# Optimization experiments

Hardware: AMD Instinct MI355X
Metric: run time of the kernel (lower is better)

## Reference

```python
import jax, jax.numpy as jnp
import numpy as np

B, N, F, H = 4, 1024, 1024, 16
D = F // H  # head_dim = 64


def setup_inputs() -> dict:
    key = jax.random.key(0)
    ks = jax.random.split(key, 12)
    s = 1.0 / np.sqrt(F)
    return {
        "feature_map": jax.random.normal(ks[0], (B, N, F), jnp.float32),
        "scene_token": jax.random.normal(ks[1], (B, F), jnp.float32),
        "relation_matrix": jax.random.normal(ks[2], (2 * N, 2 * N), jnp.float32) * 0.05,
        "Wq": jax.random.normal(ks[3], (F, F), jnp.float32) * s,
        "bq": jnp.zeros((F,), jnp.float32),
        "Wk": jax.random.normal(ks[4], (F, F), jnp.float32) * s,
        "bk": jnp.zeros((F,), jnp.float32),
        "Wv": jax.random.normal(ks[5], (F, F), jnp.float32) * s,
        "bv": jnp.zeros((F,), jnp.float32),
        "Wo": jax.random.normal(ks[6], (F, F), jnp.float32) * s,
        "bo": jnp.zeros((F,), jnp.float32),
    }


def reference(feature_map, scene_token, relation_matrix, Wq, bq, Wk, bk, Wv, bv, Wo, bo):
    b, n, f = feature_map.shape
    # scene token broadcast to n copies, concatenated -> [b, 2n, f]
    scene = jnp.broadcast_to(scene_token[:, None, :], (b, n, f))
    x = jnp.concatenate([scene, feature_map], axis=1)  # [b, 2n, f]
    q = (x @ Wq.T + bq).reshape(b, -1, H, D)
    k = (x @ Wk.T + bk).reshape(b, -1, H, D)
    v = (x @ Wv.T + bv).reshape(b, -1, H, D)
    scores = jnp.einsum("bqhd,bkhd->bhqk", q, k) / jnp.sqrt(jnp.float32(D))
    scores = scores + relation_matrix[None, None, :, :]
    weights = jax.nn.softmax(scores, axis=-1)
    attn = jnp.einsum("bhqk,bkhd->bqhd", weights, v).reshape(b, -1, f)
    return attn @ Wo.T + bo
```

## Files before the change

kernel.cpp:

```cpp
#include <hip/hip_runtime.h>
#include <hip/hip_bf16.h>
#include <cstdint>

typedef __hip_bfloat16 bf16;
typedef __attribute__((ext_vector_type(8))) short short8;
typedef __attribute__((ext_vector_type(4))) short short4v;
typedef __attribute__((ext_vector_type(4))) float f32x4;
typedef __attribute__((ext_vector_type(2))) unsigned int uint2v;

#define MFMA16(a, b, c) __builtin_amdgcn_mfma_f32_16x16x32_bf16((a), (b), (c), 0, 0, 0)

__device__ __forceinline__ void gl2lds16(const void* g, void* l) {
  __builtin_amdgcn_global_load_lds(
      (const __attribute__((address_space(1))) unsigned int*)g,
      (__attribute__((address_space(3))) unsigned int*)l,
      16, 0, 0);
}

__device__ __forceinline__ unsigned int pkcvt(float a, float b) {
  unsigned int r;
  asm("v_cvt_pk_bf16_f32 %0, %1, %2" : "=v"(r) : "v"(a), "v"(b));
  return r;
}

// ... 16 lines not shown
#endif
}

__device__ __forceinline__ uint2v plswap16(unsigned a, unsigned b) {
#if __has_builtin(__builtin_amdgcn_permlane16_swap)
  return __builtin_amdgcn_permlane16_swap(a, b, false, false);
#else
  const unsigned ax = __shfl_xor((int)a, 16), bx = __shfl_xor((int)b, 16);
  const bool hi = (threadIdx.x & 16) != 0;
  uint2v r;
  r[0] = hi ? bx : a;
  r[1] = hi ? b : ax;
  return r;
#endif
}

template <int V> struct IC { static constexpr int value = V; };

template <int WRITE_BF16, int REMAP>
__global__ __launch_bounds__(256) void gemm_bt(
    const bf16* __restrict__ A, const bf16* __restrict__ Bt,
    const float* __restrict__ bias, bf16* __restrict__ outb,
    float* __restrict__ outf, int M, int N, int K) {
  __shared__ bf16 sA[128 * 64];
  __shared__ bf16 sB[128 * 64];
  const int tid = threadIdx.x, w = tid >> 6, lane = tid & 63;
  const int n16 = lane & 15, quad = lane >> 4;
  const int mBase = blockIdx.y * 128, nBase = blockIdx.x * 128;
  const int wr = w >> 1, wc = w & 1;

  f32x4 acc[4][4];
#pragma unroll
  for (int mi = 0; mi < 4; mi++)
#pragma unroll
    for (int ni = 0; ni < 4; ni++) acc[mi][ni] = (f32x4){0.f, 0.f, 0.f, 0.f};

  const bf16* ag[4];
  const bf16* bg[4];
#pragma unroll
  for (int i = 0; i < 4; i++) {
    const int e = (i * 256 + tid) * 8;
    const int row = e >> 6, c0 = e & 63;
    const int col = c0 ^ ((row & 7) << 3);
    ag[i] = A + (size_t)(mBase + row) * K + col;
    bg[i] = Bt + (size_t)(nBase + row) * K + col;
  }
  const int u = (quad * 16) ^ ((n16 & 7) << 4);
  const int a0 = (wr * 64 + n16) * 128 + u;
// ... 6 lines not shown
#pragma unroll
    for (int i = 0; i < 4; i++) {
      gl2lds16(ag[i] + k0, sA + i * 2048 + w * 512);
      gl2lds16(bg[i] + k0, sB + i * 2048 + w * 512);
    }
    __syncthreads();

#pragma unroll
    for (int kk = 0; kk < 2; kk++) {
      short8 af[4], bfg[4];
#pragma unroll
      for (int t = 0; t < 4; t++) {
        af[t] = *(const short8*)(sAB + (a0 ^ (kk << 6)) + t * 2048);
        bfg[t] = *(const short8*)(sBB + (b0 ^ (kk << 6)) + t * 2048);
      }
#pragma unroll
      for (int mi = 0; mi < 4; mi++)
#pragma unroll
        for (int ni = 0; ni < 4; ni++)
          acc[mi][ni] = MFMA16(af[mi], bfg[ni], acc[mi][ni]);
    }
  }

#pragma unroll
  for (int mi = 0; mi < 4; mi++)
#pragma unroll
    for (int ni = 0; ni < 4; ni++)
#pragma unroll
      for (int r = 0; r < 4; r++) {
        const int row = mBase + wr * 64 + mi * 16 + quad * 4 + r;
        const int col = nBase + wc * 64 + ni * 16 + n16;
        const size_t orow =
            REMAP ? (size_t)((row >> 10) * 2048 + 1024 + (row & 1023))
                  : (size_t)row;
        const float v = acc[mi][ni][r] + bias[col];
        if (WRITE_BF16)
          outb[orow * N + col] = __float2bfloat16(v);
        else
          outf[orow * N + col] = v;
      }
}

__global__ __launch_bounds__(256) void flash_feat(
    const bf16* __restrict__ qkv, const float* __restrict__ relf,
    bf16* __restrict__ attn, const float* __restrict__ lR1) {
  constexpr int S = 2048, R3 = 3072;
  __shared__ __align__(16) char smem[32768];
  bf16* const sK = (bf16*)smem;
  char* const sVtB = smem + 16384;

  const int tid = threadIdx.x, w = tid >> 6, lane = tid & 63;
  const int n16 = lane & 15, quad = lane >> 4;
  const int bh = blockIdx.x >> 3;
  const int qt = 8 + (blockIdx.x & 7);
  const int h = bh & 15, b = bh >> 4;
  const int qb = qt * 128 + w * 32;
  const size_t rowbase = (size_t)b * S;
  const size_t krow0 = rowbase + 1024;
  const float SC = 0.125f * 1.44269504f;
  const size_t TADV = (size_t)64 * R3;

  short8 qf[2][2];
#pragma unroll
  for (int mi = 0; mi < 2; mi++) {
    const bf16* qp = qkv + (rowbase + qb + mi * 16 + n16) * R3 + h * 64;
#pragma unroll
    for (int c = 0; c < 2; c++)
      qf[mi][c] = *(const short8*)(qp + c * 32 + quad * 8);
  }

  f32x4 ot[4][2];
#pragma unroll
  for (int nc = 0; nc < 4; nc++)
#pragma unroll
    for (int mi = 0; mi < 2; mi++) ot[nc][mi] = (f32x4){0.f, 0.f, 0.f, 0.f};
  float l_lane[2] = {0.f, 0.f};

  const bf16* kg0;
  const bf16* kg1;
  {
    const int e0 = tid * 8;
    const int e1i = (256 + tid) * 8;
    const int k0r = e0 >> 6, c00 = e0 & 63;
    const int k1r = e1i >> 6, c01 = e1i & 63;
    kg0 = qkv + (krow0 + k0r) * R3 + 1024 + h * 64 + (c00 ^ ((k0r & 7) << 3));
    kg1 = qkv + (krow0 + k1r) * R3 + 1024 + h * 64 + (c01 ^ ((k1r & 7) << 3));
  }
  const int kldsoff = w * 512;

  const int kb0 = n16 * 128 + ((quad * 16) ^ ((n16 & 7) << 4));
  const int kb1 = kb0 ^ 64;
  const char* const sKB = (const char*)sK;

  const int kp = lane & 31;
  const int vd0 = w * 16 + (lane >> 5) * 8;
  const int kp4 = kp * 4;
  const bf16* vp = qkv + (krow0 + 2 * kp) * R3 + 2048 + h * 64 + vd0;

  const int vb0 = 128 * n16 + ((16 * quad) ^ ((n16 & 7) << 4));
  const int vb1 = vb0 ^ 64;

  short8 v0, v1;
  auto vstage = [&](int bufbyte) {
    const unsigned* a1 = (const unsigned*)&v1;
    const unsigned* a0 = (const unsigned*)&v0;
#pragma unroll
    for (int j = 0; j < 4; j++) {
      const unsigned lo = __builtin_amdgcn_perm(a1[j], a0[j], 0x05040100u);
      const unsigned hi = __builtin_amdgcn_perm(a1[j], a0[j], 0x07060302u);
      *(unsigned*)(sVtB + bufbyte + 128 * (vd0 + 2 * j) + (kp4 ^ ((2 * j) << 4))) = lo;
      *(unsigned*)(sVtB + bufbyte + 128 * (vd0 + 2 * j + 1) + (kp4 ^ ((2 * j + 1) << 4))) = hi;
    }
  };

  gl2lds16(kg0, sK + kldsoff);
  gl2lds16(kg1, sK + kldsoff + 2048);
  kg0 += TADV;
  kg1 += TADV;

  v0 = *(const short8*)vp;
  v1 = *(const short8*)(vp + R3);
  vstage(0);
  vp += TADV;
  v0 = *(const short8*)vp;
  v1 = *(const short8*)(vp + R3);
  vp += TADV;

  float4 rv[8];
  const float4* rpA = (const float4*)relf +
                      (size_t)(qt * 32 + 16) * 2048 + w * 512 + lane;
  const float4* rpB = rpA + 256;
#pragma unroll
  for (int j = 0; j < 4; j++) {
    rv[j] = rpA[j * 64];
    rv[4 + j] = rpB[j * 64];
  }
  rpA += 2048;
  rpB += 2048;

  auto step = [&](auto curc, bool dodma, bool dovpf) {
    constexpr int CUR = decltype(curc)::value;
    constexpr int NXT = CUR ^ 1;
    __syncthreads();

    if (dodma) {
      gl2lds16(kg0, sK + NXT * 4096 + kldsoff);
      kg0 += TADV;
      gl2lds16(kg1, sK + NXT * 4096 + kldsoff + 2048);
      kg1 += TADV;
      vstage(NXT * 8192);
    }

#pragma unroll
    for (int kc = 0; kc < 2; kc++) {
      f32x4 st[2][2];
#pragma unroll
      for (int t2 = 0; t2 < 2; t2++) {
        const int kt4 = 2 * kc + t2;
        short8 kf[2];
        kf[0] = *(const short8*)(sKB + CUR * 8192 + kt4 * 2048 + kb0);
        kf[1] = *(const short8*)(sKB + CUR * 8192 + kt4 * 2048 + kb1);
#pragma unroll
        for (int mi = 0; mi < 2; mi++) {
          f32x4 z = (f32x4){0.f, 0.f, 0.f, 0.f};
          z = MFMA16(kf[0], qf[mi][0], z);
          z = MFMA16(kf[1], qf[mi][1], z);
          st[t2][mi] = z;
        }
      }
      if (kc == 0 && dovpf) {
        v0 = *(const short8*)vp;
        v1 = *(const short8*)(vp + R3);
        vp += TADV;
      }
      short8 pb[2];
#pragma unroll
      for (int mi = 0; mi < 2; mi++) {
        float acc = 0.f;
        unsigned d[2][2];
#pragma unroll
        for (int t2 = 0; t2 < 2; t2++) {
          const float4 rr = rv[mi * 4 + 2 * kc + t2];
          float p0 = __builtin_amdgcn_exp2f(fmaf(st[t2][mi][0], SC, rr.x));
          float p1 = __builtin_amdgcn_exp2f(fmaf(st[t2][mi][1], SC, rr.y));
          float p2 = __builtin_amdgcn_exp2f(fmaf(st[t2][mi][2], SC, rr.z));
          float p3 = __builtin_amdgcn_exp2f(fmaf(st[t2][mi][3], SC, rr.w));
          acc += (p0 + p1) + (p2 + p3);
          d[t2][0] = pkcvt(p0, p1);
          d[t2][1] = pkcvt(p2, p3);
        }
        l_lane[mi] += acc;
        const uint2v e0 = plswap32(d[0][0], d[1][0]);
        const uint2v e1 = plswap32(d[0][1], d[1][1]);
        const uint2v f0 = plswap16(e0[0], e0[1]);
        const uint2v f1 = plswap16(e1[0], e1[1]);
        union { short8 s; unsigned u[4]; } P;
        P.u[0] = f0[0]; P.u[1] = f1[0]; P.u[2] = f0[1]; P.u[3] = f1[1];
        pb[mi] = P.s;
      }
      if (kc == 1 && dodma) {
#pragma unroll
        for (int j = 0; j < 4; j++) {
          rv[j] = rpA[j * 64];
          rv[4 + j] = rpB[j * 64];
        }
        rpA += 2048;
        rpB += 2048;
      }
      short8 va[4];
#pragma unroll
      for (int nc = 0; nc < 4; nc++)
        va[nc] = *(const short8*)(sVtB + CUR * 8192 + 2048 * nc +
                                  (kc ? vb1 : vb0));
#pragma unroll
      for (int nc = 0; nc < 4; nc++)
#pragma unroll
        for (int mi = 0; mi < 2; mi++)
          ot[nc][mi] = MFMA16(va[nc], pb[mi], ot[nc][mi]);
    }
  };

#pragma unroll 1
  for (int t = 0; t < 8; t++) {
    const bool g = (t < 7);
    step(IC<0>{}, true, g);
    step(IC<1>{}, g, g);
  }

  {
    const bf16* kscp = qkv + rowbase * R3 + 1024 + h * 64 + quad * 8;
    const short8 ks0 = *(const short8*)(kscp);
    const short8 ks1 = *(const short8*)(kscp + 32);
    float e1v[2];
#pragma unroll
    for (int mi = 0; mi < 2; mi++) {
      float ss = 0.f;
#pragma unroll
      for (int j = 0; j < 8; j++) {
        ss = fmaf(b2f((unsigned short)qf[mi][0][j]), b2f((unsigned short)ks0[j]), ss);
        ss = fmaf(b2f((unsigned short)qf[mi][1][j]), b2f((unsigned short)ks1[j]), ss);
      }
      ss += __shfl_xor(ss, 16);
      ss += __shfl_xor(ss, 32);
      const float lr = lR1[qb + mi * 16 + n16];
      e1v[mi] = __builtin_amdgcn_exp2f(fmaf(ss, SC, lr));
      if (quad == 0) l_lane[mi] += e1v[mi];
    }
    const bf16* vscp = qkv + rowbase * R3 + 2048 + h * 64;
#pragma unroll
    for (int nc = 0; nc < 4; nc++) {
      const int d0 = nc * 16 + quad * 4;
      const uint2 vv = *(const uint2*)(vscp + d0);
      const float w0 = b2f((unsigned short)(vv.x & 0xffff));
      const float w1 = b2f((unsigned short)(vv.x >> 16));
      const float w2 = b2f((unsigned short)(vv.y & 0xffff));
      const float w3 = b2f((unsigned short)(vv.y >> 16));
#pragma unroll
      for (int mi = 0; mi < 2; mi++) {
        ot[nc][mi][0] = fmaf(e1v[mi], w0, ot[nc][mi][0]);
        ot[nc][mi][1] = fmaf(e1v[mi], w1, ot[nc][mi][1]);
        ot[nc][mi][2] = fmaf(e1v[mi], w2, ot[nc][mi][2]);
        ot[nc][mi][3] = fmaf(e1v[mi], w3, ot[nc][mi][3]);
      }
    }
  }

  float inv[2];
#pragma unroll
  for (int mi = 0; mi < 2; mi++) {
    float l = l_lane[mi];
    l += __shfl_xor(l, 16);
    l += __shfl_xor(l, 32);
    inv[mi] = 1.0f / l;
  }
  __syncthreads();
  bf16* const sEp = (bf16*)smem + w * (32 * 72);
#pragma unroll
  for (int mi = 0; mi < 2; mi++)
#pragma unroll
    for (int nc = 0; nc < 4; nc++) {
      uint2 pk;
      pk.x = pkcvt(ot[nc][mi][0] * inv[mi], ot[nc][mi][1] * inv[mi]);
      pk.y = pkcvt(ot[nc][mi][2] * inv[mi], ot[nc][mi][3] * inv[mi]);
      *(uint2*)(&sEp[(mi * 16 + n16) * 72 + nc * 16 + quad * 4]) = pk;
    }
#pragma unroll
  for (int t = 0; t < 4; t++) {
    const int row = t * 8 + (lane >> 3);
    const int dcol = (lane & 7) * 8;
    const short8 vrow = *(const short8*)(&sEp[row * 72 + dcol]);
    *(short8*)(attn + (rowbase + qb + row) * 1024 + h * 64 + dcol) = vrow;
  }
}

__global__ __launch_bounds__(256) void flash_scene(
    const bf16* __restrict__ qkv, const float* __restrict__ relf,
    bf16* __restrict__ attn, const float* __restrict__ lR1,
    const float* __restrict__ ssf, const float* __restrict__ ssc) {
  constexpr int S = 2048, R3 = 3072;
  __shared__ __align__(16) char smem[18432];
  char* const sVtB = smem;

  const int tid = threadIdx.x, w = tid >> 6, lane = tid & 63;
  const int n16 = lane & 15, quad = lane >> 4;
  const int bh = blockIdx.x >> 3;
  const int qt = blockIdx.x & 7;
  const int h = bh & 15, b = bh >> 4;
  const int qb = qt * 128 + w * 32;
  const size_t rowbase = (size_t)b * S;
  const size_t krow0 = rowbase + 1024;
  const size_t TADV = (size_t)64 * R3;

  f32x4 ot[4][2];
#pragma unroll
  for (int nc = 0; nc < 4; nc++)
#pragma unroll
    for (int mi = 0; mi < 2; mi++) ot[nc][mi] = (f32x4){0.f, 0.f, 0.f, 0.f};
  float l_lane[2] = {0.f, 0.f};

  const int kp = lane & 31;
  const int vd0 = w * 16 + (lane >> 5) * 8;
  const int kp4 = kp * 4;
  const bf16* vp = qkv + (krow0 + 2 * kp) * R3 + 2048 + h * 64 + vd0;

  const int vb0 = 128 * n16 + ((16 * quad) ^ ((n16 & 7) << 4));
  const int vb1 = vb0 ^ 64;

  const float* ssp = ssf + (size_t)bh * 1024 + quad * 4;

  short8 v0, v1;
  auto vstage = [&](int bufbyte) {
    const unsigned* a1 = (const unsigned*)&v1;
    const unsigned* a0 = (const unsigned*)&v0;
#pragma unroll
    for (int j = 0; j < 4; j++) {
      const unsigned lo = __builtin_amdgcn_perm(a1[j], a0[j], 0x05040100u);
      const unsigned hi = __builtin_amdgcn_perm(a1[j], a0[j], 0x07060302u);
      *(unsigned*)(sVtB + bufbyte + 128 * (vd0 + 2 * j) + (kp4 ^ ((2 * j) << 4))) = lo;
      *(unsigned*)(sVtB + bufbyte + 128 * (vd0 + 2 * j + 1) + (kp4 ^ ((2 * j + 1) << 4))) = hi;
    }
  };

  v0 = *(const short8*)vp;
  v1 = *(const short8*)(vp + R3);
  vstage(0);
  vp += TADV;
  v0 = *(const short8*)vp;
  v1 = *(const short8*)(vp + R3);
  vp += TADV;

  float4 rv[8];
  const float4* rpA = (const float4*)relf +
                      (size_t)(qt * 32 + 16) * 2048 + w * 512 + lane;
  const float4* rpB = rpA + 256;
#pragma unroll
  for (int j = 0; j < 4; j++) {
    rv[j] = rpA[j * 64];
    rv[4 + j] = rpB[j * 64];
  }
  rpA += 2048;
  rpB += 2048;

  auto step = [&](auto curc, bool dodma, bool dovpf) {
    constexpr int CUR = decltype(curc)::value;
    constexpr int NXT = CUR ^ 1;
    __syncthreads();
    if (dodma) vstage(NXT * 8192);

#pragma unroll
    for (int kc = 0; kc < 2; kc++) {
      float4 ssq[2];
      ssq[0] = *(const float4*)(ssp + (2 * kc + 0) * 16);
      ssq[1] = *(const float4*)(ssp + (2 * kc + 1) * 16);
      if (kc == 0 && dovpf) {
        v0 = *(const short8*)vp;
        v1 = *(const short8*)(vp + R3);
        vp += TADV;
      }
      short8 pb[2];
#pragma unroll
      for (int mi = 0; mi < 2; mi++) {
        float acc = 0.f;
        unsigned d[2][2];
#pragma unroll
        for (int t2 = 0; t2 < 2; t2++) {
          const float4 rr = rv[mi * 4 + 2 * kc + t2];
          float p0 = __builtin_amdgcn_exp2f(ssq[t2].x + rr.x);
          float p1 = __builtin_amdgcn_exp2f(ssq[t2].y + rr.y);
          float p2 = __builtin_amdgcn_exp2f(ssq[t2].z + rr.z);
          float p3 = __builtin_amdgcn_exp2f(ssq[t2].w + rr.w);
          acc += (p0 + p1) + (p2 + p3);
          d[t2][0] = pkcvt(p0, p1);
          d[t2][1] = pkcvt(p2, p3);
        }
        l_lane[mi] += acc;
        const uint2v e0 = plswap32(d[0][0], d[1][0]);
        const uint2v e1 = plswap32(d[0][1], d[1][1]);
        const uint2v f0 = plswap16(e0[0], e0[1]);
        const uint2v f1 = plswap16(e1[0], e1[1]);
        union { short8 s; unsigned u[4]; } P;
        P.u[0] = f0[0]; P.u[1] = f1[0]; P.u[2] = f0[1]; P.u[3] = f1[1];
        pb[mi] = P.s;
      }
      if (kc == 1 && dodma) {
#pragma unroll
        for (int j = 0; j < 4; j++) {
          rv[j] = rpA[j * 64];
          rv[4 + j] = rpB[j * 64];
        }
        rpA += 2048;
        rpB += 2048;
      }
      short8 va[4];
#pragma unroll
      for (int nc = 0; nc < 4; nc++)
        va[nc] = *(const short8*)(sVtB + CUR * 8192 + 2048 * nc +
                                  (kc ? vb1 : vb0));
#pragma unroll
      for (int nc = 0; nc < 4; nc++)
#pragma unroll
        for (int mi = 0; mi < 2; mi++)
          ot[nc][mi] = MFMA16(va[nc], pb[mi], ot[nc][mi]);
    }
    ssp += 64;
  };

#pragma unroll 1
  for (int t = 0; t < 8; t++) {
    const bool g = (t < 7);
    step(IC<0>{}, true, g);
    step(IC<1>{}, g, g);
  }

  {
    const float sscv = ssc[bh];
    float e1v[2];
#pragma unroll
    for (int mi = 0; mi < 2; mi++) {
      const float lr = lR1[qb + mi * 16 + n16];
      e1v[mi] = __builtin_amdgcn_exp2f(sscv + lr);
      if (quad == 0) l_lane[mi] += e1v[mi];
    }
    const bf16* vscp = qkv + rowbase * R3 + 2048 + h * 64;
#pragma unroll
    for (int nc = 0; nc < 4; nc++) {
      const int d0 = nc * 16 + quad * 4;
      const uint2 vv = *(const uint2*)(vscp + d0);
      const float w0 = b2f((unsigned short)(vv.x & 0xffff));
      const float w1 = b2f((unsigned short)(vv.x >> 16));
      const float w2 = b2f((unsigned short)(vv.y & 0xffff));
      const float w3 = b2f((unsigned short)(vv.y >> 16));
#pragma unroll
      for (int mi = 0; mi < 2; mi++) {
        ot[nc][mi][0] = fmaf(e1v[mi], w0, ot[nc][mi][0]);
        ot[nc][mi][1] = fmaf(e1v[mi], w1, ot[nc][mi][1]);
        ot[nc][mi][2] = fmaf(e1v[mi], w2, ot[nc][mi][2]);
        ot[nc][mi][3] = fmaf(e1v[mi], w3, ot[nc][mi][3]);
      }
    }
  }

  float inv[2];
#pragma unroll
  for (int mi = 0; mi < 2; mi++) {
    float l = l_lane[mi];
    l += __shfl_xor(l, 16);
    l += __shfl_xor(l, 32);
    inv[mi] = 1.0f / l;
  }
  __syncthreads();
  bf16* const sEp = (bf16*)smem + w * (32 * 72);
#pragma unroll
  for (int mi = 0; mi < 2; mi++)
#pragma unroll
    for (int nc = 0; nc < 4; nc++) {
      uint2 pk;
      pk.x = pkcvt(ot[nc][mi][0] * inv[mi], ot[nc][mi][1] * inv[mi]);
      pk.y = pkcvt(ot[nc][mi][2] * inv[mi], ot[nc][mi][3] * inv[mi]);
      *(uint2*)(&sEp[(mi * 16 + n16) * 72 + nc * 16 + quad * 4]) = pk;
    }
#pragma unroll
  for (int t = 0; t < 4; t++) {
    const int row = t * 8 + (lane >> 3);
    const int dcol = (lane & 7) * 8;
    const short8 vrow = *(const short8*)(&sEp[row * 72 + dcol]);
    *(short8*)(attn + (rowbase + qb + row) * 1024 + h * 64 + dcol) = vrow;
  }
}

__global__ void prep_main(const float* __restrict__ fm, const float* __restrict__ Wq,
                          const float* __restrict__ Wk, const float* __restrict__ Wv,
                          const float* __restrict__ Wo, const float* __restrict__ bq,
                          const float* __restrict__ bk, const float* __restrict__ bv,
                          bf16* __restrict__ wW, bf16* __restrict__ wWo,
                          float* __restrict__ bC, bf16* __restrict__ x) {
  const int blk = blockIdx.x;
  if (blk < 4096) {
    const int sel = blk >> 10;
    const int i = (((blk & 1023) * 256) + threadIdx.x) * 4;
    const float* src = (sel == 0) ? Wq : (sel == 1) ? Wk : (sel == 2) ? Wv : Wo;
    bf16* dst = (sel < 3) ? (wW + ((size_t)sel << 20) + i) : (wWo + i);
    const float4 v = *(const float4*)(src + i);
    dst[0] = __float2bfloat16(v.x);
    dst[1] = __float2bfloat16(v.y);
    dst[2] = __float2bfloat16(v.z);
    dst[3] = __float2bfloat16(v.w);
    if (blk == 0) {
      for (int z = threadIdx.x; z < 3072; z += 256)
        bC[z] = (z < 1024) ? bq[z] : (z < 2048) ? bk[z - 1024] : bv[z - 2048];
// ... 127 lines not shown
  const float* bo    = (const float*)d_in[10];
  float* out = (float*)d_out;

  char* ws = (char*)d_ws;
  bf16* x    = (bf16*)(ws);
  float* relf = (float*)(ws);
  bf16* qkv  = (bf16*)(ws + (16u << 20));
  bf16* attn = (bf16*)(ws + (64u << 20));
  bf16* wW   = (bf16*)(ws + (80u << 20));
  bf16* wWo  = (bf16*)(ws + (86u << 20));
  float* bC  = (float*)(ws + (88u << 20));
  float* lR1 = (float*)(ws + (88u << 20) + 16384);
  bf16* sqv  = (bf16*)(ws + (88u << 20) + 32768);
  float* ssf = (float*)(ws + (88u << 20) + 65536);
  float* ssc = (float*)(ws + (88u << 20) + 65536 + 262144);

  prep_main<<<8192, 256, 0, stream>>>(fm, Wq, Wk, Wv, Wo, bq, bk, bv,
                                      wW, wWo, bC, x);
  scene_qkv<<<768, 256, 0, stream>>>(scene, wW, bC, sqv, qkv);
  gemm_bt<1, 1><<<dim3(24, 32), 256, 0, stream>>>(x, wW, bC, qkv, nullptr,
                                                  4096, 3072, 1024);
  sscomp<<<4100, 256, 0, stream>>>(qkv, sqv, ssf, ssc);
  prep_relr1<<<2048, 256, 0, stream>>>(rel, relf, lR1);
  flash_feat<<<512, 256, 0, stream>>>(qkv, relf, attn, lR1);
  flash_scene<<<512, 256, 0, stream>>>(qkv, relf, attn, lR1, ssf, ssc);
  gemm_bt<0, 0><<<dim3(8, 64), 256, 0, stream>>>(attn, wWo, bo, nullptr, out,
                                                 8192, 1024, 1024);
}
```

Measured before the change: 255.0 us.

## Stage GEMM epilogue through LDS for coalesced stores; merge flash kernels into one launch

The GEMM epilogue now writes the accumulator tile into shared memory and then stores whole rows with 16-byte vector writes, replacing scattered scalar global stores. The shared buffer is enlarged to hold the padded output tile. The feature-query and scene-query attention kernels are merged into one 1024-block launch that branches on block index. This removes one launch and its tail, and lets the two halves share the GPU at the same time. The cost is extra LDS traffic and barriers in the epilogue, plus higher register and LDS pressure in the merged kernel.

After: 260.6 us. 1.02x slower.

```diff
diff --git a/kernel.cpp b/kernel.cpp
--- a/kernel.cpp
+++ b/kernel.cpp
@@ -62,8 +62,9 @@
     const bf16* __restrict__ A, const bf16* __restrict__ Bt,
     const float* __restrict__ bias, bf16* __restrict__ outb,
     float* __restrict__ outf, int M, int N, int K) {
-  __shared__ bf16 sA[128 * 64];
-  __shared__ bf16 sB[128 * 64];
+  __shared__ __align__(16) char smemRaw[34816];
+  bf16* const sA = (bf16*)smemRaw;
+  bf16* const sB = (bf16*)(smemRaw + 16384);
   const int tid = threadIdx.x, w = tid >> 6, lane = tid & 63;
   const int n16 = lane & 15, quad = lane >> 4;
   const int mBase = blockIdx.y * 128, nBase = blockIdx.x * 128;
@@ -116,469 +117,499 @@
     }
   }
 
-#pragma unroll
-  for (int mi = 0; mi < 4; mi++)
-#pragma unroll
-    for (int ni = 0; ni < 4; ni++)
-#pragma unroll
-      for (int r = 0; r < 4; r++) {
-        const int row = mBase + wr * 64 + mi * 16 + quad * 4 + r;
-        const int col = nBase + wc * 64 + ni * 16 + n16;
-        const size_t orow =
-            REMAP ? (size_t)((row >> 10) * 2048 + 1024 + (row & 1023))
-                  : (size_t)row;
-        const float v = acc[mi][ni][r] + bias[col];
-        if (WRITE_BF16)
-          outb[orow * N + col] = __float2bfloat16(v);
-        else
-          outf[orow * N + col] = v;
-      }
-}
-
-__global__ __launch_bounds__(256) void flash_feat(
-    const bf16* __restrict__ qkv, const float* __restrict__ relf,
-    bf16* __restrict__ attn, const float* __restrict__ lR1) {
-  constexpr int S = 2048, R3 = 3072;
-  __shared__ __align__(16) char smem[32768];
-  bf16* const sK = (bf16*)smem;
-  char* const sVtB = smem + 16384;
-
-  const int tid = threadIdx.x, w = tid >> 6, lane = tid & 63;
-  const int n16 = lane & 15, quad = lane >> 4;
-  const int bh = blockIdx.x >> 3;
-  const int qt = 8 + (blockIdx.x & 7);
-  const int h = bh & 15, b = bh >> 4;
-  const int qb = qt * 128 + w * 32;
-  const size_t rowbase = (size_t)b * S;
-  const size_t krow0 = rowbase + 1024;
-  const float SC = 0.125f * 1.44269504f;
-  const size_t TADV = (size_t)64 * R3;
-
-  short8 qf[2][2];
-#pragma unroll
-  for (int mi = 0; mi < 2; mi++) {
-    const bf16* qp = qkv + (rowbase + qb + mi * 16 + n16) * R3 + h * 64;
-#pragma unroll
-    for (int c = 0; c < 2; c++)
-      qf[mi][c] = *(const short8*)(qp + c * 32 + quad * 8);
-  }
-
-  f32x4 ot[4][2];
-#pragma unroll
-  for (int nc = 0; nc < 4; nc++)
-#pragma unroll
-    for (int mi = 0; mi < 2; mi++) ot[nc][mi] = (f32x4){0.f, 0.f, 0.f, 0.f};
-  float l_lane[2] = {0.f, 0.f};
-
-  const bf16* kg0;
-  const bf16* kg1;
-  {
-    const int e0 = tid * 8;
-    const int e1i = (256 + tid) * 8;
-    const int k0r = e0 >> 6, c00 = e0 & 63;
-    const int k1r = e1i >> 6, c01 = e1i & 63;
-    kg0 = qkv + (krow0 + k0r) * R3 + 1024 + h * 64 + (c00 ^ ((k0r & 7) << 3));
-    kg1 = qkv + (krow0 + k1r) * R3 + 1024 + h * 64 + (c01 ^ ((k1r & 7) << 3));
-  }
-  const int kldsoff = w * 512;
-
-  const int kb0 = n16 * 128 + ((quad * 16) ^ ((n16 & 7) << 4));
-  const int kb1 = kb0 ^ 64;
-  const char* const sKB = (const char*)sK;
-
-  const int kp = lane & 31;
-  const int vd0 = w * 16 + (lane >> 5) * 8;
-  const int kp4 = kp * 4;
-  const bf16* vp = qkv + (krow0 + 2 * kp) * R3 + 2048 + h * 64 + vd0;
-
-  const int vb0 = 128 * n16 + ((16 * quad) ^ ((n16 & 7) << 4));
-  const int vb1 = vb0 ^ 64;
-
-  short8 v0, v1;
-  auto vstage = [&](int bufbyte) {
-    const unsigned* a1 = (const unsigned*)&v1;
-    const unsigned* a0 = (const unsigned*)&v0;
-#pragma unroll
-    for (int j = 0; j < 4; j++) {
-      const unsigned lo = __builtin_amdgcn_perm(a1[j], a0[j], 0x05040100u);
-      const unsigned hi = __builtin_amdgcn_perm(a1[j], a0[j], 0x07060302u);
-      *(unsigned*)(sVtB + bufbyte + 128 * (vd0 + 2 * j) + (kp4 ^ ((2 * j) << 4))) = lo;
-      *(unsigned*)(sVtB + bufbyte + 128 * (vd0 + 2 * j + 1) + (kp4 ^ ((2 * j + 1) << 4))) = hi;
-    }
-  };
-
-  gl2lds16(kg0, sK + kldsoff);
-  gl2lds16(kg1, sK + kldsoff + 2048);
-  kg0 += TADV;
-  kg1 += TADV;
-
-  v0 = *(const short8*)vp;
-  v1 = *(const short8*)(vp + R3);
-  vstage(0);
-  vp += TADV;
-  v0 = *(const short8*)vp;
-  v1 = *(const short8*)(vp + R3);
-  vp += TADV;
-
-  float4 rv[8];
-  const float4* rpA = (const float4*)relf +
-                      (size_t)(qt * 32 + 16) * 2048 + w * 512 + lane;
-  const float4* rpB = rpA + 256;
-#pragma unroll
-  for (int j = 0; j < 4; j++) {
-    rv[j] = rpA[j * 64];
-    rv[4 + j] = rpB[j * 64];
-  }
-  rpA += 2048;
-  rpB += 2048;
-
-  auto step = [&](auto curc, bool dodma, bool dovpf) {
-    constexpr int CUR = decltype(curc)::value;
-    constexpr int NXT = CUR ^ 1;
+  __syncthreads();
+  if (WRITE_BF16) {
+    bf16* LC = (bf16*)smemRaw;
+#pragma unroll
+    for (int mi = 0; mi < 4; mi++)
+#pragma unroll
+      for (int ni = 0; ni < 4; ni++)
+#pragma unroll
+        for (int r = 0; r < 4; r++) {
+          const int row = wr * 64 + mi * 16 + quad * 4 + r;
+          const int col = wc * 64 + ni * 16 + n16;
+          LC[row * 136 + col] = __float2bfloat16(acc[mi][ni][r] + bias[nBase + col]);
+        }
     __syncthreads();
-
-    if (dodma) {
-      gl2lds16(kg0, sK + NXT * 4096 + kldsoff);
-      kg0 += TADV;
-      gl2lds16(kg1, sK + NXT * 4096 + kldsoff + 2048);
-      kg1 += TADV;
-      vstage(NXT * 8192);
-    }
-
-#pragma unroll
-    for (int kc = 0; kc < 2; kc++) {
-      f32x4 st[2][2];
-#pragma unroll
-      for (int t2 = 0; t2 < 2; t2++) {
-        const int kt4 = 2 * kc + t2;
-        short8 kf[2];
-        kf[0] = *(const short8*)(sKB + CUR * 8192 + kt4 * 2048 + kb0);
-        kf[1] = *(const short8*)(sKB + CUR * 8192 + kt4 * 2048 + kb1);
-#pragma unroll
-        for (int mi = 0; mi < 2; mi++) {
-          f32x4 z = (f32x4){0.f, 0.f, 0.f, 0.f};
-          z = MFMA16(kf[0], qf[mi][0], z);
-          z = MFMA16(kf[1], qf[mi][1], z);
-          st[t2][mi] = z;
-        }
-      }
-      if (kc == 0 && dovpf) {
-        v0 = *(const short8*)vp;
-        v1 = *(const short8*)(vp + R3);
-        vp += TADV;
-      }
-      short8 pb[2];
-#pragma unroll
-      for (int mi = 0; mi < 2; mi++) {
-        float acc = 0.f;
-        unsigned d[2][2];
-#pragma unroll
-        for (int t2 = 0; t2 < 2; t2++) {
-          const float4 rr = rv[mi * 4 + 2 * kc + t2];
-          float p0 = __builtin_amdgcn_exp2f(fmaf(st[t2][mi][0], SC, rr.x));
-          float p1 = __builtin_amdgcn_exp2f(fmaf(st[t2][mi][1], SC, rr.y));
-          float p2 = __builtin_amdgcn_exp2f(fmaf(st[t2][mi][2], SC, rr.z));
-          float p3 = __builtin_amdgcn_exp2f(fmaf(st[t2][mi][3], SC, rr.w));
-          acc += (p0 + p1) + (p2 + p3);
-          d[t2][0] = pkcvt(p0, p1);
-          d[t2][1] = pkcvt(p2, p3);
-        }
-        l_lane[mi] += acc;
-        const uint2v e0 = plswap32(d[0][0], d[1][0]);
-        const uint2v e1 = plswap32(d[0][1], d[1][1]);
-        const uint2v f0 = plswap16(e0[0], e0[1]);
-        const uint2v f1 = plswap16(e1[0], e1[1]);
-        union { short8 s; unsigned u[4]; } P;
-        P.u[0] = f0[0]; P.u[1] = f1[0]; P.u[2] = f0[1]; P.u[3] = f1[1];
-        pb[mi] = P.s;
-      }
-      if (kc == 1 && dodma) {
-#pragma unroll
-        for (int j = 0; j < 4; j++) {
-          rv[j] = rpA[j * 64];
-          rv[4 + j] = rpB[j * 64];
-        }
-        rpA += 2048;
-        rpB += 2048;
-      }
-      short8 va[4];
-#pragma unroll
-      for (int nc = 0; nc < 4; nc++)
-        va[nc] = *(const short8*)(sVtB + CUR * 8192 + 2048 * nc +
-                                  (kc ? vb1 : vb0));
-#pragma unroll
-      for (int nc = 0; nc < 4; nc++)
-#pragma unroll
-        for (int mi = 0; mi < 2; mi++)
-          ot[nc][mi] = MFMA16(va[nc], pb[mi], ot[nc][mi]);
-    }
-  };
-
-#pragma unroll 1
-  for (int t = 0; t < 8; t++) {
-    const bool g = (t < 7);
-    step(IC<0>{}, true, g);
-    step(IC<1>{}, g, g);
-  }
-
-  {
-    const bf16* kscp = qkv + rowbase * R3 + 1024 + h * 64 + quad * 8;
-    const short8 ks0 = *(const short8*)(kscp);
-    const short8 ks1 = *(const short8*)(kscp + 32);
-    float e1v[2];
-#pragma unroll
-    for (int mi = 0; mi < 2; mi++) {
-      float ss = 0.f;
-#pragma unroll
-      for (int j = 0; j < 8; j++) {
-        ss = fmaf(b2f((unsigned short)qf[mi][0][j]), b2f((unsigned short)ks0[j]), ss);
-        ss = fmaf(b2f((unsigned short)qf[mi][1][j]), b2f((unsigned short)ks1[j]), ss);
-      }
-      ss += __shfl_xor(ss, 16);
-      ss += __shfl_xor(ss, 32);
-      const float lr = lR1[qb + mi * 16 + n16];
-      e1v[mi] = __builtin_amdgcn_exp2f(fmaf(ss, SC, lr));
-      if (quad == 0) l_lane[mi] += e1v[mi];
-    }
-    const bf16* vscp = qkv + rowbase * R3 + 2048 + h * 64;
-#pragma unroll
-    for (int nc = 0; nc < 4; nc++) {
-      const int d0 = nc * 16 + quad * 4;
-      const uint2 vv = *(const uint2*)(vscp + d0);
-      const float w0 = b2f((unsigned short)(vv.x & 0xffff));
-      const float w1 = b2f((unsigned short)(vv.x >> 16));
-      const float w2 = b2f((unsigned short)(vv.y & 0xffff));
-      const float w3 = b2f((unsigned short)(vv.y >> 16));
-#pragma unroll
-      for (int mi = 0; mi < 2; mi++) {
-        ot[nc][mi][0] = fmaf(e1v[mi], w0, ot[nc][mi][0]);
-        ot[nc][mi][1] = fmaf(e1v[mi], w1, ot[nc][mi][1]);
-        ot[nc][mi][2] = fmaf(e1v[mi], w2, ot[nc][mi][2]);
-        ot[nc][mi][3] = fmaf(e1v[mi], w3, ot[nc][mi][3]);
-      }
-    }
-  }
-
-  float inv[2];
-#pragma unroll
-  for (int mi = 0; mi < 2; mi++) {
-    float l = l_lane[mi];
-    l += __shfl_xor(l, 16);
-    l += __shfl_xor(l, 32);
-    inv[mi] = 1.0f / l;
-  }
-  __syncthreads();
-  bf16* const sEp = (bf16*)smem + w * (32 * 72);
-#pragma unroll
-  for (int mi = 0; mi < 2; mi++)
-#pragma unroll
-    for (int nc = 0; nc < 4; nc++) {
-      uint2 pk;
-      pk.x = pkcvt(ot[nc][mi][0] * inv[mi], ot[nc][mi][1] * inv[mi]);
-      pk.y = pkcvt(ot[nc][mi][2] * inv[mi], ot[nc][mi][3] * inv[mi]);
-      *(uint2*)(&sEp[(mi * 16 + n16) * 72 + nc * 16 + quad * 4]) = pk;
-    }
-#pragma unroll
-  for (int t = 0; t < 4; t++) {
-    const int row = t * 8 + (lane >> 3);
-    const int dcol = (lane & 7) * 8;
-    const short8 vrow = *(const short8*)(&sEp[row * 72 + dcol]);
-    *(short8*)(attn + (rowbase + qb + row) * 1024 + h * 64 + dcol) = vrow;
-  }
-}
-
-__global__ __launch_bounds__(256) void flash_scene(
+#pragma unroll
+    for (int i = 0; i < 8; i++) {
+      const int row = i * 16 + (tid >> 4);
+      const int c8 = (tid & 15) * 8;
+      const short8 vv = *(const short8*)(LC + row * 136 + c8);
+      const int grow = mBase + row;
+      const size_t orow = REMAP
+                              ? (size_t)((grow >> 10) * 2048 + 1024 + (grow & 1023))
+                              : (size_t)grow;
+      *(short8*)(outb + orow * N + nBase + c8) = vv;
+    }
+  } else {
+    float* LC = (float*)smemRaw;
+#pragma unroll
+    for (int half = 0; half < 2; half++) {
+      if (wr == half) {
+#pragma unroll
+        for (int mi = 0; mi < 4; mi++)
+#pragma unroll
+          for (int ni = 0; ni < 4; ni++)
+#pragma unroll
+            for (int r = 0; r < 4; r++) {
+              const int row = mi * 16 + quad * 4 + r;
+              const int col = wc * 64 + ni * 16 + n16;
+              LC[row * 132 + col] = acc[mi][ni][r] + bias[nBase + col];
+            }
+      }
+      __syncthreads();
+#pragma unroll
+      for (int i = 0; i < 8; i++) {
+        const int row = i * 8 + (tid >> 5);
+        const int c4 = (tid & 31) * 4;
+        const float4 vv = *(const float4*)(LC + row * 132 + c4);
+        const int grow = mBase + half * 64 + row;
+        *(float4*)(outf + (size_t)grow * N + nBase + c4) = vv;
+      }
+      __syncthreads();
+    }
+  }
+}
+
+__global__ __launch_bounds__(256) void flash_all(
     const bf16* __restrict__ qkv, const float* __restrict__ relf,
     bf16* __restrict__ attn, const float* __restrict__ lR1,
     const float* __restrict__ ssf, const float* __restrict__ ssc) {
   constexpr int S = 2048, R3 = 3072;
-  __shared__ __align__(16) char smem[18432];
-  char* const sVtB = smem;
+  __shared__ __align__(16) char smem[32768];
 
   const int tid = threadIdx.x, w = tid >> 6, lane = tid & 63;
   const int n16 = lane & 15, quad = lane >> 4;
-  const int bh = blockIdx.x >> 3;
-  const int qt = blockIdx.x & 7;
-  const int h = bh & 15, b = bh >> 4;
-  const int qb = qt * 128 + w * 32;
-  const size_t rowbase = (size_t)b * S;
-  const size_t krow0 = rowbase + 1024;
+  const float SC = 0.125f * 1.44269504f;
   const size_t TADV = (size_t)64 * R3;
 
-  f32x4 ot[4][2];
-#pragma unroll
-  for (int nc = 0; nc < 4; nc++)
-#pragma unroll
-    for (int mi = 0; mi < 2; mi++) ot[nc][mi] = (f32x4){0.f, 0.f, 0.f, 0.f};
-  float l_lane[2] = {0.f, 0.f};
-
-  const int kp = lane & 31;
-  const int vd0 = w * 16 + (lane >> 5) * 8;
-  const int kp4 = kp * 4;
-  const bf16* vp = qkv + (krow0 + 2 * kp) * R3 + 2048 + h * 64 + vd0;
-
-  const int vb0 = 128 * n16 + ((16 * quad) ^ ((n16 & 7) << 4));
-  const int vb1 = vb0 ^ 64;
-
-  const float* ssp = ssf + (size_t)bh * 1024 + quad * 4;
-
-  short8 v0, v1;
-  auto vstage = [&](int bufbyte) {
-    const unsigned* a1 = (const unsigned*)&v1;
-    const unsigned* a0 = (const unsigned*)&v0;
+  if (blockIdx.x < 512) {
+    bf16* const sK = (bf16*)smem;
+    char* const sVtB = smem + 16384;
+    const int bh = blockIdx.x >> 3;
+    const int qt = 8 + (blockIdx.x & 7);
+    const int h = bh & 15, b = bh >> 4;
+    const int qb = qt * 128 + w * 32;
+    const size_t rowbase = (size_t)b * S;
+    const size_t krow0 = rowbase + 1024;
+
+    short8 qf[2][2];
+#pragma unroll
+    for (int mi = 0; mi < 2; mi++) {
+      const bf16* qp = qkv + (rowbase + qb + mi * 16 + n16) * R3 + h * 64;
+#pragma unroll
+      for (int c = 0; c < 2; c++)
+        qf[mi][c] = *(const short8*)(qp + c * 32 + quad * 8);
+    }
+
+    f32x4 ot[4][2];
+#pragma unroll
+    for (int nc = 0; nc < 4; nc++)
+#pragma unroll
+      for (int mi = 0; mi < 2; mi++) ot[nc][mi] = (f32x4){0.f, 0.f, 0.f, 0.f};
+    float l_lane[2] = {0.f, 0.f};
+
+    const bf16* kg0;
+    const bf16* kg1;
+    {
+      const int e0 = tid * 8;
+      const int e1i = (256 + tid) * 8;
+      const int k0r = e0 >> 6, c00 = e0 & 63;
+      const int k1r = e1i >> 6, c01 = e1i & 63;
+      kg0 = qkv + (krow0 + k0r) * R3 + 1024 + h * 64 + (c00 ^ ((k0r & 7) << 3));
+      kg1 = qkv + (krow0 + k1r) * R3 + 1024 + h * 64 + (c01 ^ ((k1r & 7) << 3));
+    }
+    const int kldsoff = w * 512;
+
+    const int kb0 = n16 * 128 + ((quad * 16) ^ ((n16 & 7) << 4));
+    const int kb1 = kb0 ^ 64;
+    const char* const sKB = (const char*)sK;
+
+    const int kp = lane & 31;
+    const int vd0 = w * 16 + (lane >> 5) * 8;
+    const int kp4 = kp * 4;
+    const bf16* vp = qkv + (krow0 + 2 * kp) * R3 + 2048 + h * 64 + vd0;
+
+    const int vb0 = 128 * n16 + ((16 * quad) ^ ((n16 & 7) << 4));
+    const int vb1 = vb0 ^ 64;
+
+    short8 v0, v1;
+    auto vstage = [&](int bufbyte) {
+      const unsigned* a1 = (const unsigned*)&v1;
+      const unsigned* a0 = (const unsigned*)&v0;
+#pragma unroll
+      for (int j = 0; j < 4; j++) {
+        const unsigned lo = __builtin_amdgcn_perm(a1[j], a0[j], 0x05040100u);
+        const unsigned hi = __builtin_amdgcn_perm(a1[j], a0[j], 0x07060302u);
+        *(unsigned*)(sVtB + bufbyte + 128 * (vd0 + 2 * j) + (kp4 ^ ((2 * j) << 4))) = lo;
+        *(unsigned*)(sVtB + bufbyte + 128 * (vd0 + 2 * j + 1) + (kp4 ^ ((2 * j + 1) << 4))) = hi;
+      }
+    };
+
+    gl2lds16(kg0, sK + kldsoff);
+    gl2lds16(kg1, sK + kldsoff + 2048);
+    kg0 += TADV;
+    kg1 += TADV;
+
+    v0 = *(const short8*)vp;
+    v1 = *(const short8*)(vp + R3);
+    vstage(0);
+    vp += TADV;
+    v0 = *(const short8*)vp;
+    v1 = *(const short8*)(vp + R3);
+    vp += TADV;
+
+    float4 rv[8];
+    const float4* rpA = (const float4*)relf +
+                        (size_t)(qt * 32 + 16) * 2048 + w * 512 + lane;
+    const float4* rpB = rpA + 256;
 #pragma unroll
     for (int j = 0; j < 4; j++) {
-      const unsigned lo = __builtin_amdgcn_perm(a1[j], a0[j], 0x05040100u);
-      const unsigned hi = __builtin_amdgcn_perm(a1[j], a0[j], 0x07060302u);
-      *(unsigned*)(sVtB + bufbyte + 128 * (vd0 + 2 * j) + (kp4 ^ ((2 * j) << 4))) = lo;
-      *(unsigned*)(sVtB + bufbyte + 128 * (vd0 + 2 * j + 1) + (kp4 ^ ((2 * j + 1) << 4))) = hi;
-    }
-  };
-
-  v0 = *(const short8*)vp;
-  v1 = *(const short8*)(vp + R3);
-  vstage(0);
-  vp += TADV;
-  v0 = *(const short8*)vp;
-  v1 = *(const short8*)(vp + R3);
-  vp += TADV;
-
-  float4 rv[8];
-  const float4* rpA = (const float4*)relf +
-                      (size_t)(qt * 32 + 16) * 2048 + w * 512 + lane;
-  const float4* rpB = rpA + 256;
-#pragma unroll
-  for (int j = 0; j < 4; j++) {
-    rv[j] = rpA[j * 64];
-    rv[4 + j] = rpB[j * 64];
-  }
-  rpA += 2048;
-  rpB += 2048;
-
-  auto step = [&](auto curc, bool dodma, bool dovpf) {
-    constexpr int CUR = decltype(curc)::value;
-    constexpr int NXT = CUR ^ 1;
+      rv[j] = rpA[j * 64];
+      rv[4 + j] = rpB[j * 64];
+    }
+    rpA += 2048;
+    rpB += 2048;
+
+    auto step = [&](auto curc, bool dodma, bool dovpf) {
+      constexpr int CUR = decltype(curc)::value;
+      constexpr int NXT = CUR ^ 1;
+      __syncthreads();
+
+      if (dodma) {
+        gl2lds16(kg0, sK + NXT * 4096 + kldsoff);
+        kg0 += TADV;
+        gl2lds16(kg1, sK + NXT * 4096 + kldsoff + 2048);
+        kg1 += TADV;
+        vstage(NXT * 8192);
+      }
+
+#pragma unroll
+      for (int kc = 0; kc < 2; kc++) {
+        f32x4 st[2][2];
+#pragma unroll
+        for (int t2 = 0; t2 < 2; t2++) {
+          const int kt4 = 2 * kc + t2;
+          short8 kf[2];
+          kf[0] = *(const short8*)(sKB + CUR * 8192 + kt4 * 2048 + kb0);
+          kf[1] = *(const short8*)(sKB + CUR * 8192 + kt4 * 2048 + kb1);
+#pragma unroll
+          for (int mi = 0; mi < 2; mi++) {
+            f32x4 z = (f32x4){0.f, 0.f, 0.f, 0.f};
+            z = MFMA16(kf[0], qf[mi][0], z);
+            z = MFMA16(kf[1], qf[mi][1], z);
+            st[t2][mi] = z;
+          }
+        }
+        if (kc == 0 && dovpf) {
+          v0 = *(const short8*)vp;
+          v1 = *(const short8*)(vp + R3);
+          vp += TADV;
+        }
+        short8 pb[2];
+#pragma unroll
+        for (int mi = 0; mi < 2; mi++) {
+          float acc = 0.f;
+          unsigned d[2][2];
+#pragma unroll
+          for (int t2 = 0; t2 < 2; t2++) {
+            const float4 rr = rv[mi * 4 + 2 * kc + t2];
+            float p0 = __builtin_amdgcn_exp2f(fmaf(st[t2][mi][0], SC, rr.x));
+            float p1 = __builtin_amdgcn_exp2f(fmaf(st[t2][mi][1], SC, rr.y));
+            float p2 = __builtin_amdgcn_exp2f(fmaf(st[t2][mi][2], SC, rr.z));
+            float p3 = __builtin_amdgcn_exp2f(fmaf(st[t2][mi][3], SC, rr.w));
+            acc += (p0 + p1) + (p2 + p3);
+            d[t2][0] = pkcvt(p0, p1);
+            d[t2][1] = pkcvt(p2, p3);
+          }
+          l_lane[mi] += acc;
+          const uint2v e0 = plswap32(d[0][0], d[1][0]);
+          const uint2v e1 = plswap32(d[0][1], d[1][1]);
+          const uint2v f0 = plswap16(e0[0], e0[1]);
+          const uint2v f1 = plswap16(e1[0], e1[1]);
+          union { short8 s; unsigned u[4]; } P;
+          P.u[0] = f0[0]; P.u[1] = f1[0]; P.u[2] = f0[1]; P.u[3] = f1[1];
+          pb[mi] = P.s;
+        }
+        if (kc == 1 && dodma) {
+#pragma unroll
+          for (int j = 0; j < 4; j++) {
+            rv[j] = rpA[j * 64];
+            rv[4 + j] = rpB[j * 64];
+          }
+          rpA += 2048;
+          rpB += 2048;
+        }
+        short8 va[4];
+#pragma unroll
+        for (int nc = 0; nc < 4; nc++)
+          va[nc] = *(const short8*)(sVtB + CUR * 8192 + 2048 * nc +
+                                    (kc ? vb1 : vb0));
+#pragma unroll
+        for (int nc = 0; nc < 4; nc++)
+#pragma unroll
+          for (int mi = 0; mi < 2; mi++)
+            ot[nc][mi] = MFMA16(va[nc], pb[mi], ot[nc][mi]);
+      }
+    };
+
+#pragma unroll 1
+    for (int t = 0; t < 8; t++) {
+      const bool g = (t < 7);
+      step(IC<0>{}, true, g);
+      step(IC<1>{}, g, g);
+    }
+
+    {
+      const bf16* kscp = qkv + rowbase * R3 + 1024 + h * 64 + quad * 8;
+      const short8 ks0 = *(const short8*)(kscp);
+      const short8 ks1 = *(const short8*)(kscp + 32);
+      float e1v[2];
+#pragma unroll
+      for (int mi = 0; mi < 2; mi++) {
+        float ss = 0.f;
+#pragma unroll
+        for (int j = 0; j < 8; j++) {
+          ss = fmaf(b2f((unsigned short)qf[mi][0][j]), b2f((unsigned short)ks0[j]), ss);
+          ss = fmaf(b2f((unsigned short)qf[mi][1][j]), b2f((unsigned short)ks1[j]), ss);
+        }
+        ss += __shfl_xor(ss, 16);
+        ss += __shfl_xor(ss, 32);
+        const float lr = lR1[qb + mi * 16 + n16];
+        e1v[mi] = __builtin_amdgcn_exp2f(fmaf(ss, SC, lr));
+        if (quad == 0) l_lane[mi] += e1v[mi];
+      }
+      const bf16* vscp = qkv + rowbase * R3 + 2048 + h * 64;
+#pragma unroll
+      for (int nc = 0; nc < 4; nc++) {
+        const int d0 = nc * 16 + quad * 4;
+        const uint2 vv = *(const uint2*)(vscp + d0);
+        const float w0 = b2f((unsigned short)(vv.x & 0xffff));
+        const float w1 = b2f((unsigned short)(vv.x >> 16));
+        const float w2 = b2f((unsigned short)(vv.y & 0xffff));
+        const float w3 = b2f((unsigned short)(vv.y >> 16));
+#pragma unroll
+        for (int mi = 0; mi < 2; mi++) {
+          ot[nc][mi][0] = fmaf(e1v[mi], w0, ot[nc][mi][0]);
+          ot[nc][mi][1] = fmaf(e1v[mi], w1, ot[nc][mi][1]);
+          ot[nc][mi][2] = fmaf(e1v[mi], w2, ot[nc][mi][2]);
+          ot[nc][mi][3] = fmaf(e1v[mi], w3, ot[nc][mi][3]);
+        }
+      }
+    }
+
+    float inv[2];
+#pragma unroll
+    for (int mi = 0; mi < 2; mi++) {
+      float l = l_lane[mi];
+      l += __shfl_xor(l, 16);
+      l += __shfl_xor(l, 32);
+      inv[mi] = 1.0f / l;
+    }
     __syncthreads();
-    if (dodma) vstage(NXT * 8192);
-
-#pragma unroll
-    for (int kc = 0; kc < 2; kc++) {
-      float4 ssq[2];
-      ssq[0] = *(const float4*)(ssp + (2 * kc + 0) * 16);
-      ssq[1] = *(const float4*)(ssp + (2 * kc + 1) * 16);
-      if (kc == 0 && dovpf) {
-        v0 = *(const short8*)vp;
-        v1 = *(const short8*)(vp + R3);
-        vp += TADV;
-      }
-      short8 pb[2];
+    bf16* const sEp = (bf16*)smem + w * (32 * 72);
+#pragma unroll
+    for (int mi = 0; mi < 2; mi++)
+#pragma unroll
+      for (int nc = 0; nc < 4; nc++) {
+        uint2 pk;
+        pk.x = pkcvt(ot[nc][mi][0] * inv[mi], ot[nc][mi][1] * inv[mi]);
+        pk.y = pkcvt(ot[nc][mi][2] * inv[mi], ot[nc][mi][3] * inv[mi]);
+        *(uint2*)(&sEp[(mi * 16 + n16) * 72 + nc * 16 + quad * 4]) = pk;
+      }
+#pragma unroll
+    for (int t = 0; t < 4; t++) {
+      const int row = t * 8 + (lane >> 3);
+      const int dcol = (lane & 7) * 8;
+      const short8 vrow = *(const short8*)(&sEp[row * 72 + dcol]);
+      *(short8*)(attn + (rowbase + qb + row) * 1024 + h * 64 + dcol) = vrow;
+    }
+  } else {
+    char* const sVtB = smem;
+    const int m = blockIdx.x - 512;
+    const int bh = m >> 3;
+    const int qt = m & 7;
+    const int h = bh & 15, b = bh >> 4;
+    const int qb = qt * 128 + w * 32;
+    const size_t rowbase = (size_t)b * S;
+    const size_t krow0 = rowbase + 1024;
+
+    f32x4 ot[4][2];
+#pragma unroll
+    for (int nc = 0; nc < 4; nc++)
+#pragma unroll
+      for (int mi = 0; mi < 2; mi++) ot[nc][mi] = (f32x4){0.f, 0.f, 0.f, 0.f};
+    float l_lane[2] = {0.f, 0.f};
+
+    const int kp = lane & 31;
+    const int vd0 = w * 16 + (lane >> 5) * 8;
+    const int kp4 = kp * 4;
+    const bf16* vp = qkv + (krow0 + 2 * kp) * R3 + 2048 + h * 64 + vd0;
+
+    const int vb0 = 128 * n16 + ((16 * quad) ^ ((n16 & 7) << 4));
+    const int vb1 = vb0 ^ 64;
+
+    const float* ssp = ssf + (size_t)bh * 1024 + quad * 4;
+
+    short8 v0, v1;
+    auto vstage = [&](int bufbyte) {
+      const unsigned* a1 = (const unsigned*)&v1;
+      const unsigned* a0 = (const unsigned*)&v0;
+#pragma unroll
+      for (int j = 0; j < 4; j++) {
+        const unsigned lo = __builtin_amdgcn_perm(a1[j], a0[j], 0x05040100u);
+        const unsigned hi = __builtin_amdgcn_perm(a1[j], a0[j], 0x07060302u);
+        *(unsigned*)(sVtB + bufbyte + 128 * (vd0 + 2 * j) + (kp4 ^ ((2 * j) << 4))) = lo;
+        *(unsigned*)(sVtB + bufbyte + 128 * (vd0 + 2 * j + 1) + (kp4 ^ ((2 * j + 1) << 4))) = hi;
+      }
+    };
+
+    v0 = *(const short8*)vp;
+    v1 = *(const short8*)(vp + R3);
+    vstage(0);
+    vp += TADV;
+    v0 = *(const short8*)vp;
+    v1 = *(const short8*)(vp + R3);
+    vp += TADV;
+
+    float4 rv[8];
+    const float4* rpA = (const float4*)relf +
+                        (size_t)(qt * 32 + 16) * 2048 + w * 512 + lane;
+    const float4* rpB = rpA + 256;
+#pragma unroll
+    for (int j = 0; j < 4; j++) {
+      rv[j] = rpA[j * 64];
+      rv[4 + j] = rpB[j * 64];
+    }
+    rpA += 2048;
+    rpB += 2048;
+
+    auto step = [&](auto curc, bool dodma, bool dovpf) {
+      constexpr int CUR = decltype(curc)::value;
+      constexpr int NXT = CUR ^ 1;
+      __syncthreads();
+      if (dodma) vstage(NXT * 8192);
+
+#pragma unroll
+      for (int kc = 0; kc < 2; kc++) {
+        float4 ssq[2];
+        ssq[0] = *(const float4*)(ssp + (2 * kc + 0) * 16);
+        ssq[1] = *(const float4*)(ssp + (2 * kc + 1) * 16);
+        if (kc == 0 && dovpf) {
+          v0 = *(const short8*)vp;
+          v1 = *(const short8*)(vp + R3);
+          vp += TADV;
+        }
+        short8 pb[2];
+#pragma unroll
+        for (int mi = 0; mi < 2; mi++) {
+          float acc = 0.f;
+          unsigned d[2][2];
+#pragma unroll
+          for (int t2 = 0; t2 < 2; t2++) {
+            const float4 rr = rv[mi * 4 + 2 * kc + t2];
+            float p0 = __builtin_amdgcn_exp2f(ssq[t2].x + rr.x);
+            float p1 = __builtin_amdgcn_exp2f(ssq[t2].y + rr.y);
+            float p2 = __builtin_amdgcn_exp2f(ssq[t2].z + rr.z);
+            float p3 = __builtin_amdgcn_exp2f(ssq[t2].w + rr.w);
+            acc += (p0 + p1) + (p2 + p3);
+            d[t2][0] = pkcvt(p0, p1);
+            d[t2][1] = pkcvt(p2, p3);
+          }
+          l_lane[mi] += acc;
+          const uint2v e0 = plswap32(d[0][0], d[1][0]);
+          const uint2v e1 = plswap32(d[0][1], d[1][1]);
+          const uint2v f0 = plswap16(e0[0], e0[1]);
+          const uint2v f1 = plswap16(e1[0], e1[1]);
+          union { short8 s; unsigned u[4]; } P;
+          P.u[0] = f0[0]; P.u[1] = f1[0]; P.u[2] = f0[1]; P.u[3] = f1[1];
+          pb[mi] = P.s;
+        }
+        if (kc == 1 && dodma) {
+#pragma unroll
+          for (int j = 0; j < 4; j++) {
+            rv[j] = rpA[j * 64];
+            rv[4 + j] = rpB[j * 64];
+          }
+          rpA += 2048;
+          rpB += 2048;
+        }
+        short8 va[4];
+#pragma unroll
+        for (int nc = 0; nc < 4; nc++)
+          va[nc] = *(const short8*)(sVtB + CUR * 8192 + 2048 * nc +
+                                    (kc ? vb1 : vb0));
+#pragma unroll
+        for (int nc = 0; nc < 4; nc++)
+#pragma unroll
+          for (int mi = 0; mi < 2; mi++)
+            ot[nc][mi] = MFMA16(va[nc], pb[mi], ot[nc][mi]);
+      }
+      ssp += 64;
+    };
+
+#pragma unroll 1
+    for (int t = 0; t < 8; t++) {
+      const bool g = (t < 7);
+      step(IC<0>{}, true, g);
+      step(IC<1>{}, g, g);
+    }
+
+    {
+      const float sscv = ssc[bh];
+      float e1v[2];
 #pragma unroll
       for (int mi = 0; mi < 2; mi++) {
-        float acc = 0.f;
-        unsigned d[2][2];
-#pragma unroll
-        for (int t2 = 0; t2 < 2; t2++) {
-          const float4 rr = rv[mi * 4 + 2 * kc + t2];
-          float p0 = __builtin_amdgcn_exp2f(ssq[t2].x + rr.x);
-          float p1 = __builtin_amdgcn_exp2f(ssq[t2].y + rr.y);
-          float p2 = __builtin_amdgcn_exp2f(ssq[t2].z + rr.z);
-          float p3 = __builtin_amdgcn_exp2f(ssq[t2].w + rr.w);
-          acc += (p0 + p1) + (p2 + p3);
-          d[t2][0] = pkcvt(p0, p1);
-          d[t2][1] = pkcvt(p2, p3);
-        }
-        l_lane[mi] += acc;
-        const uint2v e0 = plswap32(d[0][0], d[1][0]);
-        const uint2v e1 = plswap32(d[0][1], d[1][1]);
-        const uint2v f0 = plswap16(e0[0], e0[1]);
-        const uint2v f1 = plswap16(e1[0], e1[1]);
-        union { short8 s; unsigned u[4]; } P;
-        P.u[0] = f0[0]; P.u[1] = f1[0]; P.u[2] = f0[1]; P.u[3] = f1[1];
-        pb[mi] = P.s;
-      }
-      if (kc == 1 && dodma) {
-#pragma unroll
-        for (int j = 0; j < 4; j++) {
-          rv[j] = rpA[j * 64];
-          rv[4 + j] = rpB[j * 64];
-        }
-        rpA += 2048;
-        rpB += 2048;
-      }
-      short8 va[4];
-#pragma unroll
-      for (int nc = 0; nc < 4; nc++)
-        va[nc] = *(const short8*)(sVtB + CUR * 8192 + 2048 * nc +
-                                  (kc ? vb1 : vb0));
-#pragma unroll
-      for (int nc = 0; nc < 4; nc++)
-#pragma unroll
-        for (int mi = 0; mi < 2; mi++)
-          ot[nc][mi] = MFMA16(va[nc], pb[mi], ot[nc][mi]);
-    }
-    ssp += 64;
-  };
-
-#pragma unroll 1
-  for (int t = 0; t < 8; t++) {
-    const bool g = (t < 7);
-    step(IC<0>{}, true, g);
-    step(IC<1>{}, g, g);
-  }
-
-  {
-    const float sscv = ssc[bh];
-    float e1v[2];
+        const float lr = lR1[qb + mi * 16 + n16];
+        e1v[mi] = __builtin_amdgcn_exp2f(sscv + lr);
+        if (quad == 0) l_lane[mi] += e1v[mi];
+      }
+      const bf16* vscp = qkv + rowbase * R3 + 2048 + h * 64;
+#pragma unroll
+      for (int nc = 0; nc < 4; nc++) {
+        const int d0 = nc * 16 + quad * 4;
+        const uint2 vv = *(const uint2*)(vscp + d0);
+        const float w0 = b2f((unsigned short)(vv.x & 0xffff));
+        const float w1 = b2f((unsigned short)(vv.x >> 16));
+        const float w2 = b2f((unsigned short)(vv.y & 0xffff));
+        const float w3 = b2f((unsigned short)(vv.y >> 16));
+#pragma unroll
+        for (int mi = 0; mi < 2; mi++) {
+          ot[nc][mi][0] = fmaf(e1v[mi], w0, ot[nc][mi][0]);
+          ot[nc][mi][1] = fmaf(e1v[mi], w1, ot[nc][mi][1]);
+          ot[nc][mi][2] = fmaf(e1v[mi], w2, ot[nc][mi][2]);
+          ot[nc][mi][3] = fmaf(e1v[mi], w3, ot[nc][mi][3]);
+        }
+      }
+    }
+
+    float inv[2];
 #pragma unroll
     for (int mi = 0; mi < 2; mi++) {
-      const float lr = lR1[qb + mi * 16 + n16];
-      e1v[mi] = __builtin_amdgcn_exp2f(sscv + lr);
-      if (quad == 0) l_lane[mi] += e1v[mi];
-    }
-    const bf16* vscp = qkv + rowbase * R3 + 2048 + h * 64;
-#pragma unroll
-    for (int nc = 0; nc < 4; nc++) {
-      const int d0 = nc * 16 + quad * 4;
-      const uint2 vv = *(const uint2*)(vscp + d0);
-      const float w0 = b2f((unsigned short)(vv.x & 0xffff));
-      const float w1 = b2f((unsigned short)(vv.x >> 16));
-      const float w2 = b2f((unsigned short)(vv.y & 0xffff));
-      const float w3 = b2f((unsigned short)(vv.y >> 16));
-#pragma unroll
-      for (int mi = 0; mi < 2; mi++) {
-        ot[nc][mi][0] = fmaf(e1v[mi], w0, ot[nc][mi][0]);
-        ot[nc][mi][1] = fmaf(e1v[mi], w1, ot[nc][mi][1]);
-        ot[nc][mi][2] = fmaf(e1v[mi], w2, ot[nc][mi][2]);
-        ot[nc][mi][3] = fmaf(e1v[mi], w3, ot[nc][mi][3]);
-      }
-    }
-  }
-
-  float inv[2];
-#pragma unroll
-  for (int mi = 0; mi < 2; mi++) {
-    float l = l_lane[mi];
-    l += __shfl_xor(l, 16);
-    l += __shfl_xor(l, 32);
-    inv[mi] = 1.0f / l;
-  }
-  __syncthreads();
-  bf16* const sEp = (bf16*)smem + w * (32 * 72);
-#pragma unroll
-  for (int mi = 0; mi < 2; mi++)
-#pragma unroll
-    for (int nc = 0; nc < 4; nc++) {
-      uint2 pk;
-      pk.x = pkcvt(ot[nc][mi][0] * inv[mi], ot[nc][mi][1] * inv[mi]);
-      pk.y = pkcvt(ot[nc][mi][2] * inv[mi], ot[nc][mi][3] * inv[mi]);
-      *(uint2*)(&sEp[(mi * 16 + n16) * 72 + nc * 16 + quad * 4]) = pk;
-    }
-#pragma unroll
-  for (int t = 0; t < 4; t++) {
-    const int row = t * 8 + (lane >> 3);
-    const int dcol = (lane & 7) * 8;
-    const short8 vrow = *(const short8*)(&sEp[row * 72 + dcol]);
-    *(short8*)(attn + (rowbase + qb + row) * 1024 + h * 64 + dcol) = vrow;
+      float l = l_lane[mi];
+      l += __shfl_xor(l, 16);
+      l += __shfl_xor(l, 32);
+      inv[mi] = 1.0f / l;
+    }
+    __syncthreads();
+    bf16* const sEp = (bf16*)smem + w * (32 * 72);
+#pragma unroll
+    for (int mi = 0; mi < 2; mi++)
+#pragma unroll
+      for (int nc = 0; nc < 4; nc++) {
+        uint2 pk;
+        pk.x = pkcvt(ot[nc][mi][0] * inv[mi], ot[nc][mi][1] * inv[mi]);
+        pk.y = pkcvt(ot[nc][mi][2] * inv[mi], ot[nc][mi][3] * inv[mi]);
+        *(uint2*)(&sEp[(mi * 16 + n16) * 72 + nc * 16 + quad * 4]) = pk;
+      }
+#pragma unroll
+    for (int t = 0; t < 4; t++) {
+      const int row = t * 8 + (lane >> 3);
+      const int dcol = (lane & 7) * 8;
+      const short8 vrow = *(const short8*)(&sEp[row * 72 + dcol]);
+      *(short8*)(attn + (rowbase + qb + row) * 1024 + h * 64 + dcol) = vrow;
+    }
   }
 }
 
@@ -752,8 +783,7 @@
                                                   4096, 3072, 1024);
   sscomp<<<4100, 256, 0, stream>>>(qkv, sqv, ssf, ssc);
   prep_relr1<<<2048, 256, 0, stream>>>(rel, relf, lR1);
-  flash_feat<<<512, 256, 0, stream>>>(qkv, relf, attn, lR1);
-  flash_scene<<<512, 256, 0, stream>>>(qkv, relf, attn, lR1, ssf, ssc);
+  flash_all<<<1024, 256, 0, stream>>>(qkv, relf, attn, lR1, ssf, ssc);
   gemm_bt<0, 0><<<dim3(8, 64), 256, 0, stream>>>(attn, wWo, bo, nullptr, out,
                                                  8192, 1024, 1024);
 }
```
